# Performance work log

Hardware: AMD Instinct MI355X
Metric: run time of the kernel (lower is better)

The kernel has to match this reference:

```python
import jax, jax.numpy as jnp
import numpy as np

B, NZ, L = 8, 16, 512
E, DM, NH, HD = 256, 512, 16, 32
FF, NL, E1D, PDIM, PMAX = 1024, 8, 32, 64, 24
EPS_LN = 1e-5
EPS_D = 1e-12


def _ln(x, g, b):
    m = jnp.mean(x, axis=-1, keepdims=True)
    v = jnp.mean((x - m) ** 2, axis=-1, keepdims=True)
    return (x - m) / jnp.sqrt(v + EPS_LN) * g + b


def setup_inputs() -> dict:
    key = jax.random.key(0)
    ks = iter(jax.random.split(key, 32))
    rn = lambda shape, fan: jax.random.normal(next(ks), shape, jnp.float32) / np.float32(np.sqrt(fan))
    inp = {
        "z": jax.random.normal(next(ks), (B, NZ, L), jnp.float32),
        "x": jax.random.uniform(next(ks), (B, 20, L), jnp.float32),
        # embeddings
        "pos_table": rn((2 * PMAX + 1, PDIM), 1.0),
        "aa_table": rn((20, E1D), 1.0),
        # embed_x: Linear(nz,E), relu, Linear(E,E)
        "ex_w1": rn((NZ, E), NZ), "ex_b1": jnp.zeros((E,), jnp.float32),
        "ex_w2": rn((E, E), E), "ex_b2": jnp.zeros((E,), jnp.float32),
        # per-layer stacked params
        "Wq": rn((NL, E, DM), E), "Wk": rn((NL, E, DM), E), "Wv": rn((NL, E, DM), E),
        "Wo": rn((NL, DM, E), DM), "bo": jnp.zeros((NL, E), jnp.float32),
        "W2d": rn((NL, PDIM, NH), PDIM), "b2d": jnp.zeros((NL, NH), jnp.float32),
        "W1": rn((NL, E + E1D, FF), E + E1D), "b1": jnp.zeros((NL, FF), jnp.float32),
        "W2": rn((NL, FF, E), FF), "b2": jnp.zeros((NL, E), jnp.float32),
        "g1": jnp.ones((NL, E), jnp.float32), "be1": jnp.zeros((NL, E), jnp.float32),
        "g2": jnp.ones((NL, E), jnp.float32), "be2": jnp.zeros((NL, E), jnp.float32),
        # mlp_3d: Linear(E,E), relu, Linear(E,3)
        "m3_w1": rn((E, E), E), "m3_b1": jnp.zeros((E,), jnp.float32),
        "m3_w2": rn((E, 3), E), "m3_b2": jnp.zeros((3,), jnp.float32),
    }
    return inp


def reference(z, x, pos_table, aa_table, ex_w1, ex_b1, ex_w2, ex_b2,
              Wq, Wk, Wv, Wo, bo, W2d, b2d, W1, b1, W2, b2,
              g1, be1, g2, be2, m3_w1, m3_b1, m3_w2, m3_b2):
    Bn, _, Ln = z.shape
    h = jnp.transpose(z, (0, 2, 1))  # (B, L, nz)
    # relative-position bins: argmin over integer bins == clip to [-PMAX, PMAX]
    rel = jnp.arange(Ln)[None, :] - jnp.arange(Ln)[:, None]
    bins = jnp.clip(rel, -PMAX, PMAX) + PMAX
    pe = pos_table[bins]  # (L, L, PDIM), batch-replicated
    e_aa = aa_table[jnp.argmax(x, axis=1)]  # (B, L, E1D)
    # embed_x MLP
    h = jax.nn.relu(h @ ex_w1 + ex_b1) @ ex_w2 + ex_b2  # (B, L, E)
    scale = np.float32(1.0 / np.sqrt(DM))  # dp_attn_norm='d_model'
    for i in range(NL):
        q = (h @ Wq[i]).reshape(Bn, Ln, NH, HD) * scale
        k = (h @ Wk[i]).reshape(Bn, Ln, NH, HD)
        v = (h @ Wv[i]).reshape(Bn, Ln, NH, HD)
        # learned pairwise bias: mlp_2d then transpose(1,3).transpose(2,3) -> bias[h,i,j] = out[i,j,h]
        bias = jnp.einsum('lmp,ph->hlm', pe, W2d[i]) + b2d[i][:, None, None]
        scores = jnp.einsum('blhd,bmhd->bhlm', q, k) + bias[None]
        attn = jax.nn.softmax(scores, axis=-1)
        o = jnp.einsum('bhlm,bmhd->blhd', attn, v).reshape(Bn, Ln, DM)
        h = _ln(h + (o @ Wo[i] + bo[i]), g1[i], be1[i])
        um = jnp.concatenate([h, e_aa], axis=-1)  # (B, L, E+E1D)
        s2 = jax.nn.relu(um @ W1[i] + b1[i]) @ W2[i] + b2[i]
        h = _ln(h + s2, g2[i], be2[i])
    r = jax.nn.relu(h @ m3_w1 + m3_b1) @ m3_w2 + m3_b2  # (B, L, 3)
    # distance map (get_coords=False path)
    d = jnp.sqrt(jnp.sum((r[:, None, :, :] - r[:, :, None, :]) ** 2, axis=-1) + EPS_D)
    return d  # (B, L, L)
```

## Files before the change

kernel.cpp:

```cpp
#include <hip/hip_runtime.h>
#include <math.h>

constexpr int Bn = 8, NZ = 16, Ln = 512;
constexpr int E = 256, DM = 512, NH = 16, HD = 32;
constexpr int FF = 1024, NL = 8, E1D = 32, PDIM = 64, PMAX = 24;
constexpr int ROWS = Bn * Ln;
constexpr float QSCALE = 0.04419417382415922f;

typedef __attribute__((ext_vector_type(8))) short bf16x8;
typedef __attribute__((ext_vector_type(4))) float floatx4;

__device__ inline unsigned short f2b(float f) {
  union { float f; unsigned u; } v; v.f = f;
  unsigned r = (v.u + 0x7FFF + ((v.u >> 16) & 1)) >> 16;
  return (unsigned short)r;
}
__device__ inline float b2f(unsigned short u) {
  union { unsigned u; float f; } v; v.u = ((unsigned)u) << 16; return v.f;
}

__device__ inline void gll16(const void* g, void* l) {
  __builtin_amdgcn_global_load_lds(
      (const __attribute__((address_space(1))) void*)g,
      (__attribute__((address_space(3))) void*)l, 16, 0, 0);
}

template<int CTRL>
__device__ inline float fmax_dpp(float x) {
  int y = __builtin_amdgcn_update_dpp(0, __float_as_int(x), CTRL, 0xf, 0xf, true);
  return fmaxf(x, __int_as_float(y));
}

template<int CTRL>
__device__ inline float fadd_dpp(float x) {
  int y = __builtin_amdgcn_update_dpp(0, __float_as_int(x), CTRL, 0xf, 0xf, true);
  return x + __int_as_float(y);
}

__global__ __launch_bounds__(256) void transpose_qkv(
    const float* __restrict__ Wq, const float* __restrict__ Wk,
    const float* __restrict__ Wv, unsigned short* __restrict__ qkvT)
{
  __shared__ float t[32][33];
  int zb = blockIdx.z;
  int which = zb / NL, l = zb % NL;
  const float* s = (which == 0 ? Wq : which == 1 ? Wk : Wv) + (size_t)l * E * DM;
  unsigned short* d = qkvT + (size_t)l * 3 * DM * E + (size_t)which * DM * E;
  int c0 = blockIdx.x * 32, r0 = blockIdx.y * 32;
  int tx = threadIdx.x & 31, ty = threadIdx.x >> 5;
  #pragma unroll
  for (int i = 0; i < 4; ++i)
    t[ty + i * 8][tx] = s[(size_t)(r0 + ty + i * 8) * DM + c0 + tx];
  __syncthreads();
  #pragma unroll
  for (int i = 0; i < 4; ++i)
    d[(size_t)(c0 + ty + i * 8) * E + r0 + tx] = f2b(t[tx][ty + i * 8]);
}

__global__ __launch_bounds__(256) void transpose_bf16(
    const float* __restrict__ src, unsigned short* __restrict__ dst,
    int R, int C, size_t sls, size_t dls)
{
  __shared__ float t[32][33];
  int l = blockIdx.z;
  int c0 = blockIdx.x * 32, r0 = blockIdx.y * 32;
  int tx = threadIdx.x & 31, ty = threadIdx.x >> 5;
  const float* s = src + (size_t)l * sls;
  unsigned short* d = dst + (size_t)l * dls;
  #pragma unroll
  for (int i = 0; i < 4; ++i)
    t[ty + i * 8][tx] = s[(size_t)(r0 + ty + i * 8) * C + c0 + tx];
  __syncthreads();
  #pragma unroll
  for (int i = 0; i < 4; ++i)
    d[(size_t)(c0 + ty + i * 8) * R + r0 + tx] = f2b(t[tx][ty + i * 8]);
}

__global__ __launch_bounds__(256) void embed1_kernel(
    const float* __restrict__ z, const float* __restrict__ x,
    const float* __restrict__ aa,
    const float* __restrict__ w1, const float* __restrict__ b1,
    float* __restrict__ t0, unsigned short* __restrict__ umb)
{
  int row = blockIdx.x;
  int b = row >> 9, l = row & (Ln - 1);
  int t = threadIdx.x;
  __shared__ float zs[NZ];
  __shared__ int am_s;
  if (t < NZ) zs[t] = z[((size_t)b * NZ + t) * Ln + l];
  if (t == 0) {
    const float* xp = x + (size_t)b * 20 * Ln + l;
    int am = 0; float bv = xp[0];
    for (int c = 1; c < 20; ++c) { float vv = xp[(size_t)c * Ln]; if (vv > bv) { bv = vv; am = c; } }
    am_s = am;
  }
  __syncthreads();
  float a1 = b1[t];
  #pragma unroll
  for (int nz = 0; nz < NZ; ++nz) a1 += zs[nz] * w1[nz * E + t];
  t0[(size_t)row * E + t] = fmaxf(a1, 0.f);
  if (t < E1D) umb[(size_t)row * (E + E1D) + E + t] = f2b(aa[am_s * E1D + t]);
}

__global__ __launch_bounds__(256) void bias_kernel(
    const float* __restrict__ pos, const float* __restrict__ W2d,
    const float* __restrict__ b2d, float* __restrict__ bias49)
{
  int layer = blockIdx.x;
  for (int idx = threadIdx.x; idx < NH * 49; idx += 256) {
    int hh = idx / 49, bin = idx % 49;
    float acc = b2d[layer * NH + hh];
    for (int p = 0; p < PDIM; ++p)
      acc += pos[bin * PDIM + p] * W2d[((size_t)layer * PDIM + p) * NH + hh];
    bias49[(size_t)layer * NH * 49 + hh * 49 + bin] = acc;
  }
}

template<int BM, int BN, int BK, bool BIAS, bool RELU, bool OUTBF16, bool QKV>
__global__ __launch_bounds__(256) void gemm_mfma(
    const unsigned short* __restrict__ A, const unsigned short* __restrict__ Bt,
    const float* __restrict__ bias,
    float* __restrict__ Cf, unsigned short* __restrict__ Cb, int N, int K)
{
  constexpr int MT = BM / 32, NT = BN / 32;
  const int tid = threadIdx.x;
  const int wave = tid >> 6, ln = tid & 63;
  const int quad = ln >> 4, l16 = ln & 15;
  const int wm = wave >> 1, wn = wave & 1;
  const int m0 = blockIdx.y * BM, n0 = blockIdx.x * BN;

  floatx4 acc[MT][NT] = {};

  if constexpr (BK == 32) {
    __shared__ __align__(16) unsigned short As[2][BM][32];
    __shared__ __align__(16) unsigned short Bs[2][BN][32];
    const int lrow = ln >> 2, chunk = ln & 3;
    const int schunk = chunk ^ ((lrow >> 1) & 3);
    const unsigned short* aSrc = A + (size_t)(m0 + wave * 16 + lrow) * K + schunk * 8;
    const unsigned short* bSrc = Bt + (size_t)(n0 + wave * 16 + lrow) * K + schunk * 8;
    const int rkey = (l16 >> 1) & 3;
    const int nk = K >> 5;

    #pragma unroll
    for (int it = 0; it < BM / 64; ++it)
      gll16(aSrc + (size_t)it * 64 * K, &As[0][it * 64 + wave * 16][0]);
    #pragma unroll
    for (int it = 0; it < BN / 64; ++it)
      gll16(bSrc + (size_t)it * 64 * K, &Bs[0][it * 64 + wave * 16][0]);

    for (int t = 0; t < nk; ++t) {
      const int cur = t & 1;
      __syncthreads();
      if (t + 1 < nk) {
        const int kb = (t + 1) << 5;
        #pragma unroll
        for (int it = 0; it < BM / 64; ++it)
          gll16(aSrc + (size_t)it * 64 * K + kb, &As[cur ^ 1][it * 64 + wave * 16][0]);
        #pragma unroll
        for (int it = 0; it < BN / 64; ++it)
          gll16(bSrc + (size_t)it * 64 * K + kb, &Bs[cur ^ 1][it * 64 + wave * 16][0]);
      }
      bf16x8 af[MT], bfr[NT];
      #pragma unroll
      for (int i = 0; i < MT; ++i)
        af[i] = *(const bf16x8*)&As[cur][wm * (BM / 2) + i * 16 + l16][(quad ^ rkey) * 8];
      #pragma unroll
      for (int j = 0; j < NT; ++j)
        bfr[j] = *(const bf16x8*)&Bs[cur][wn * (BN / 2) + j * 16 + l16][(quad ^ rkey) * 8];
      #pragma unroll
      for (int i = 0; i < MT; ++i)
        #pragma unroll
        for (int j = 0; j < NT; ++j)
          acc[i][j] = __builtin_amdgcn_mfma_f32_16x16x32_bf16(af[i], bfr[j], acc[i][j], 0, 0, 0);
    }
  } else {
    __shared__ __align__(16) unsigned short As[BM][128];
    __shared__ __align__(16) unsigned short Bs[BN][128];
    const int lrow = ln >> 4, chunk = ln & 15;
    const int key = wave * 4 + lrow;
    const int schunk = chunk ^ key;
    const unsigned short* aSrc = A + (size_t)(m0 + key) * K + schunk * 8;
    const unsigned short* bSrc = Bt + (size_t)(n0 + key) * K + schunk * 8;

    for (int kb = 0; kb < K; kb += 128) {
      __syncthreads();
      #pragma unroll
      for (int it = 0; it < BM / 16; ++it)
        gll16(aSrc + (size_t)(it * 16) * K + kb, &As[it * 16 + wave * 4][0]);
      #pragma unroll
      for (int it = 0; it < BN / 16; ++it)
        gll16(bSrc + (size_t)(it * 16) * K + kb, &Bs[it * 16 + wave * 4][0]);
      __syncthreads();
      #pragma unroll
      for (int kc = 0; kc < 4; ++kc) {
        bf16x8 af[MT], bfr[NT];
        #pragma unroll
        for (int i = 0; i < MT; ++i)
          af[i] = *(const bf16x8*)&As[wm * (BM / 2) + i * 16 + l16][(((kc * 4 + quad) ^ l16) * 8)];
        #pragma unroll
        for (int j = 0; j < NT; ++j)
          bfr[j] = *(const bf16x8*)&Bs[wn * (BN / 2) + j * 16 + l16][(((kc * 4 + quad) ^ l16) * 8)];
        #pragma unroll
        for (int i = 0; i < MT; ++i)
          #pragma unroll
          for (int j = 0; j < NT; ++j)
            acc[i][j] = __builtin_amdgcn_mfma_f32_16x16x32_bf16(af[i], bfr[j], acc[i][j], 0, 0, 0);
      }
    }
  }

  #pragma unroll
  for (int i = 0; i < MT; ++i)
    #pragma unroll
    for (int j = 0; j < NT; ++j) {
      int col = n0 + wn * (BN / 2) + j * 16 + l16;
      float bv = BIAS ? bias[col] : 0.f;
      float sc = QKV ? (col < 512 ? QSCALE : 1.f) : 1.f;
      #pragma unroll
      for (int r = 0; r < 4; ++r) {
        int rowg = m0 + wm * (BM / 2) + i * 16 + quad * 4 + r;
        float v = acc[i][j][r] * sc + bv;
        if (RELU) v = fmaxf(v, 0.f);
        if (OUTBF16) Cb[(size_t)rowg * N + col] = f2b(v);
        else Cf[(size_t)rowg * N + col] = v;
      }
    }
}

__global__ __launch_bounds__(256) void gemm_ln(
    const unsigned short* __restrict__ A, const unsigned short* __restrict__ Bt,
    const float* __restrict__ bias, float* __restrict__ h,
    const float* __restrict__ g, const float* __restrict__ be,
    unsigned short* __restrict__ outb, int bstride, int K)
{
  __shared__ __align__(16) unsigned short As[2][16][128];
  __shared__ __align__(16) unsigned short Bs[2][256][128];
  __shared__ __align__(16) float vtile[16][260];
  const int tid = threadIdx.x;
  const int w = tid >> 6, ln = tid & 63;
  const int quad = ln >> 4, l16 = ln & 15;
  const int m0 = blockIdx.x * 16;
  const int lrow = ln >> 4, chunk = ln & 15;
  const int key = w * 4 + lrow;
  const int schunk = chunk ^ key;
  const unsigned short* aSrc = A + (size_t)(m0 + key) * K + schunk * 8;
  const unsigned short* bSrc = Bt + (size_t)key * K + schunk * 8;

  floatx4 acc[4] = {};
  const int nk = K >> 7;

  gll16(aSrc, &As[0][w * 4][0]);
  #pragma unroll
  for (int it = 0; it < 16; ++it)
    gll16(bSrc + (size_t)(it * 16) * K, &Bs[0][it * 16 + w * 4][0]);

  for (int t = 0; t < nk; ++t) {
    const int cur = t & 1;
    __syncthreads();
    if (t + 1 < nk) {
      const int kb = (t + 1) << 7;
      gll16(aSrc + kb, &As[cur ^ 1][w * 4][0]);
      #pragma unroll
      for (int it = 0; it < 16; ++it)
        gll16(bSrc + (size_t)(it * 16) * K + kb, &Bs[cur ^ 1][it * 16 + w * 4][0]);
    }
    #pragma unroll
    for (int kc = 0; kc < 4; ++kc) {
      bf16x8 af = *(const bf16x8*)&As[cur][l16][(((kc * 4 + quad) ^ l16) * 8)];
      #pragma unroll
      for (int nt = 0; nt < 4; ++nt) {
        bf16x8 bf = *(const bf16x8*)&Bs[cur][w * 64 + nt * 16 + l16][(((kc * 4 + quad) ^ l16) * 8)];
        acc[nt] = __builtin_amdgcn_mfma_f32_16x16x32_bf16(af, bf, acc[nt], 0, 0, 0);
      }
    }
  }

  #pragma unroll
  for (int nt = 0; nt < 4; ++nt) {
    int col = w * 64 + nt * 16 + l16;
    float bv = bias[col];
    #pragma unroll
    for (int r = 0; r < 4; ++r) {
      int row = quad * 4 + r;
      vtile[row][col] = acc[nt][r] + bv + h[(size_t)(m0 + row) * E + col];
    }
  }
  __syncthreads();

  const int c0 = ln * 4;
  #pragma unroll
  for (int rr = 0; rr < 4; ++rr) {
    const int lr = w * 4 + rr;
    float4 v = *(const float4*)&vtile[lr][c0];
    float s = v.x + v.y + v.z + v.w;
    float s2 = v.x * v.x + v.y * v.y + v.z * v.z + v.w * v.w;
    s  = fadd_dpp<0xB1>(s);   s  = fadd_dpp<0x4E>(s);
    s2 = fadd_dpp<0xB1>(s2);  s2 = fadd_dpp<0x4E>(s2);
    #pragma unroll
    for (int off = 4; off < 64; off <<= 1) {
      s += __shfl_xor(s, off, 64);
      s2 += __shfl_xor(s2, off, 64);
    }
    const float mean = s * (1.f / E);
    const float rstd = rsqrtf(s2 * (1.f / E) - mean * mean + 1e-5f);
    const float4 gv = *(const float4*)(g + c0);
    const float4 bv = *(const float4*)(be + c0);
    float4 y;
    y.x = (v.x - mean) * rstd * gv.x + bv.x;
    y.y = (v.y - mean) * rstd * gv.y + bv.y;
    y.z = (v.z - mean) * rstd * gv.z + bv.z;
    y.w = (v.w - mean) * rstd * gv.w + bv.w;
    const size_t row = (size_t)(m0 + lr);
    *(float4*)(h + row * E + c0) = y;
    ushort4 yb;
    yb.x = f2b(y.x); yb.y = f2b(y.y); yb.z = f2b(y.z); yb.w = f2b(y.w);
    *(ushort4*)(outb + row * (size_t)bstride + c0) = yb;
  }
}

__global__ __launch_bounds__(256) void attn_kernel(
    const unsigned short* __restrict__ qkv, const float* __restrict__ bias49,
    unsigned short* __restrict__ o)
{
  const int id = blockIdx.x;
  const int bh = ((id >> 6) << 3) | (id & 7);
  const int i0 = ((id >> 3) & 7) * 64;
  const int b = bh >> 4, hh = bh & 15;
  const int tid = threadIdx.x;
  const int wave = tid >> 6, ln = tid & 63;
  const int quad = ln >> 4, l16 = ln & 15;

  __shared__ __align__(16) unsigned short Kt[2][64][40];
  __shared__ __align__(16) unsigned short Vt[2][32][72];
  __shared__ __align__(16) unsigned short Pw[4][2][16][72];
  __shared__ float bsh[49];

  if (tid < 49) bsh[tid] = bias49[hh * 49 + tid];

  const unsigned short* qkvb = qkv + (size_t)b * Ln * 1536;

  const int qrow = i0 + wave * 16 + l16;
  const bf16x8 qf = *(const bf16x8*)(qkvb + (size_t)qrow * 1536 + hh * 32 + quad * 8);

  float m[4], l[4];
  #pragma unroll
  for (int r = 0; r < 4; ++r) { m[r] = -1e30f; l[r] = 0.f; }
  floatx4 acc_o[2] = {};

  const int krow = tid >> 2, kch = (tid & 3) * 8;
  const int vkey = tid & 63, vch = (tid >> 6) * 8;
  const unsigned short* kp = qkvb + (size_t)krow * 1536 + 512 + hh * 32 + kch;
  const unsigned short* vp = qkvb + (size_t)vkey * 1536 + 1024 + hh * 32 + vch;

  float4 kreg = *(const float4*)kp;
  bf16x8 vreg = *(const bf16x8*)vp;

  for (int jt = 0; jt < 8; ++jt) {
    const int j0 = jt * 64;
    const int cur = jt & 1;
    *(float4*)&Kt[cur][krow][kch] = kreg;
    #pragma unroll
    for (int i = 0; i < 8; ++i) Vt[cur][vch + i][vkey] = (unsigned short)vreg[i];
    __syncthreads();
    if (jt < 7) {
      kreg = *(const float4*)(kp + (size_t)(j0 + 64) * 1536);
      vreg = *(const bf16x8*)(vp + (size_t)(j0 + 64) * 1536);
    }

    floatx4 s4[4];
    #pragma unroll
    for (int t = 0; t < 4; ++t) {
      bf16x8 kf = *(const bf16x8*)&Kt[cur][16 * t + l16][quad * 8];
      s4[t] = __builtin_amdgcn_mfma_f32_16x16x32_bf16(qf, kf, (floatx4){0.f, 0.f, 0.f, 0.f}, 0, 0, 0);
    }
    const int relmin = j0 - (i0 + 63), relmax = j0 + 63 - i0;
    if (relmin >= PMAX) {
      float bc = bsh[48];
      #pragma unroll
      for (int t = 0; t < 4; ++t)
        #pragma unroll
        for (int r = 0; r < 4; ++r) s4[t][r] += bc;
    } else if (relmax <= -PMAX) {
      float bc = bsh[0];
      #pragma unroll
      for (int t = 0; t < 4; ++t)
        #pragma unroll
        for (int r = 0; r < 4; ++r) s4[t][r] += bc;
    } else {
      const int base_rel = (j0 + l16) - (i0 + wave * 16 + quad * 4);
      #pragma unroll
      for (int t = 0; t < 4; ++t)
        #pragma unroll
        for (int r = 0; r < 4; ++r) {
          int rel = base_rel + 16 * t - r;
          rel = rel < -PMAX ? -PMAX : (rel > PMAX ? PMAX : rel);
          s4[t][r] += bsh[rel + PMAX];
        }
    }

    float mloc[4], alpha[4], psum[4];
    #pragma unroll
    for (int r = 0; r < 4; ++r) {
      mloc[r] = fmaxf(fmaxf(s4[0][r], s4[1][r]), fmaxf(s4[2][r], s4[3][r]));
      mloc[r] = fmax_dpp<0xB1>(mloc[r]);
      mloc[r] = fmax_dpp<0x4E>(mloc[r]);
      mloc[r] = fmax_dpp<0x124>(mloc[r]);
      mloc[r] = fmax_dpp<0x128>(mloc[r]);
      float mnew = fmaxf(m[r], mloc[r]);
      alpha[r] = __expf(m[r] - mnew);
      m[r] = mnew;
      psum[r] = 0.f;
    }
    #pragma unroll
    for (int t = 0; t < 4; ++t)
      #pragma unroll
      for (int r = 0; r < 4; ++r) {
        float p = __expf(s4[t][r] - m[r]);
        s4[t][r] = p;
        psum[r] += p;
      }
    #pragma unroll
    for (int r = 0; r < 4; ++r) {
      psum[r] = fadd_dpp<0xB1>(psum[r]);
      psum[r] = fadd_dpp<0x4E>(psum[r]);
      #pragma unroll
      for (int off = 4; off < 16; off <<= 1)
        psum[r] += __shfl_xor(psum[r], off, 64);
      l[r] = l[r] * alpha[r] + psum[r];
      acc_o[0][r] *= alpha[r];
      acc_o[1][r] *= alpha[r];
    }

    #pragma unroll
    for (int t = 0; t < 4; ++t)
      #pragma unroll
      for (int r = 0; r < 4; ++r) {
        float p = s4[t][r];
        unsigned short hi = f2b(p);
        unsigned short lo = f2b(p - b2f(hi));
        Pw[wave][0][quad * 4 + r][16 * t + l16] = hi;
        Pw[wave][1][quad * 4 + r][16 * t + l16] = lo;
      }

    #pragma unroll
    for (int kh = 0; kh < 2; ++kh) {
      bf16x8 phi = *(const bf16x8*)&Pw[wave][0][l16][kh * 32 + quad * 8];
      bf16x8 plo = *(const bf16x8*)&Pw[wave][1][l16][kh * 32 + quad * 8];
      #pragma unroll
      for (int nt = 0; nt < 2; ++nt) {
        bf16x8 vf = *(const bf16x8*)&Vt[cur][nt * 16 + l16][kh * 32 + quad * 8];
        acc_o[nt] = __builtin_amdgcn_mfma_f32_16x16x32_bf16(phi, vf, acc_o[nt], 0, 0, 0);
        acc_o[nt] = __builtin_amdgcn_mfma_f32_16x16x32_bf16(plo, vf, acc_o[nt], 0, 0, 0);
      }
    }
  }

  #pragma unroll
  for (int r = 0; r < 4; ++r) {
    float inv = 1.f / l[r];
    size_t rowg = (size_t)b * Ln + i0 + wave * 16 + quad * 4 + r;
    #pragma unroll
    for (int nt = 0; nt < 2; ++nt)
      o[rowg * 512 + hh * 32 + nt * 16 + l16] = f2b(acc_o[nt][r] * inv);
  }
}

template<bool RELU, bool BIAS, bool MIRROR>
__global__ __launch_bounds__(256) void gemm64f(
    const float* __restrict__ A, const float* __restrict__ B,
    const float* __restrict__ bias, float* __restrict__ C,
    unsigned short* __restrict__ mir, int N, int K)
{
  __shared__ __align__(16) float As[16][64];
  __shared__ __align__(16) float Bss[16][68];
  const int tid = threadIdx.x;
  const int tx = tid & 15, ty = tid >> 4;
  const int m0 = blockIdx.y * 64, n0 = blockIdx.x * 64;
  const int arow = tid >> 2, acol = (tid & 3) * 4;
  const int brow = tid >> 6, bcol = tid & 63;
  float acc[4][4] = {};
  for (int kb = 0; kb < K; kb += 16) {
    __syncthreads();
    float4 av = *(const float4*)(A + (size_t)(m0 + arow) * K + kb + acol);
    As[acol + 0][arow] = av.x; As[acol + 1][arow] = av.y;
    As[acol + 2][arow] = av.z; As[acol + 3][arow] = av.w;
    #pragma unroll
    for (int kk = 0; kk < 4; ++kk)
      Bss[brow + kk * 4][bcol] = B[(size_t)(kb + brow + kk * 4) * N + n0 + bcol];
    __syncthreads();
    #pragma unroll
    for (int k = 0; k < 16; ++k) {
      float4 a = *(const float4*)&As[k][4 * ty];
      float4 b = *(const float4*)&Bss[k][4 * tx];
      float av4[4] = {a.x, a.y, a.z, a.w};
      float bv4[4] = {b.x, b.y, b.z, b.w};
      #pragma unroll
      for (int ii = 0; ii < 4; ++ii)
        #pragma unroll
        for (int jj = 0; jj < 4; ++jj)
          acc[ii][jj] += av4[ii] * bv4[jj];
    }
  }
  #pragma unroll
  for (int ii = 0; ii < 4; ++ii) {
    size_t row = (size_t)m0 + 4 * ty + ii;
    int col = n0 + 4 * tx;
    float4 vv;
    vv.x = acc[ii][0]; vv.y = acc[ii][1]; vv.z = acc[ii][2]; vv.w = acc[ii][3];
    if (BIAS) {
      float4 bb = *(const float4*)(bias + col);
      vv.x += bb.x; vv.y += bb.y; vv.z += bb.z; vv.w += bb.w;
    }
    if (RELU) {
      vv.x = fmaxf(vv.x, 0.f); vv.y = fmaxf(vv.y, 0.f);
      vv.z = fmaxf(vv.z, 0.f); vv.w = fmaxf(vv.w, 0.f);
    }
    *(float4*)(C + row * N + col) = vv;
    if (MIRROR) {
      ushort4 mv;
      mv.x = f2b(vv.x); mv.y = f2b(vv.y); mv.z = f2b(vv.z); mv.w = f2b(vv.w);
      *(ushort4*)(mir + row * N + col) = mv;
    }
  }
}

__global__ __launch_bounds__(256) void final_r_kernel(
    const float* __restrict__ t1, const float* __restrict__ w2,
    const float* __restrict__ b2, float* __restrict__ r)
{
  int row = blockIdx.x, t = threadIdx.x;
  float xv = t1[(size_t)row * E + t];
  float p0 = xv * w2[t * 3 + 0];
  float p1 = xv * w2[t * 3 + 1];
  float p2 = xv * w2[t * 3 + 2];
  #pragma unroll
  for (int off = 32; off > 0; off >>= 1) {
    p0 += __shfl_down(p0, off, 64);
    p1 += __shfl_down(p1, off, 64);
    p2 += __shfl_down(p2, off, 64);
  }
  __shared__ float red[4][3];
  if ((t & 63) == 0) { int w = t >> 6; red[w][0] = p0; red[w][1] = p1; red[w][2] = p2; }
  __syncthreads();
  if (t < 3)
    r[(size_t)row * 3 + t] = red[0][t] + red[1][t] + red[2][t] + red[3][t] + b2[t];
}

__global__ __launch_bounds__(512) void dist_kernel(
    const float* __restrict__ r, float* __restrict__ out)
{
  int bi = blockIdx.x;
  int j = threadIdx.x;
  int b = bi >> 9;
  float x0 = r[(size_t)bi * 3 + 0];
  float y0 = r[(size_t)bi * 3 + 1];
  float z0 = r[(size_t)bi * 3 + 2];
  const float* rj = r + ((size_t)b * Ln + j) * 3;
  float dx = rj[0] - x0, dy = rj[1] - y0, dz = rj[2] - z0;
  out[(size_t)bi * Ln + j] = sqrtf(dx * dx + dy * dy + dz * dz + 1e-12f);
}

extern "C" void kernel_launch(void* const* d_in, const int* in_sizes, int n_in,
                              void* d_out, int out_size, void* d_ws, size_t ws_size,
                              hipStream_t stream)
{
  const float* z     = (const float*)d_in[0];
  const float* x     = (const float*)d_in[1];
  const float* pos   = (const float*)d_in[2];
  const float* aa    = (const float*)d_in[3];
  const float* ex_w1 = (const float*)d_in[4];
  const float* ex_b1 = (const float*)d_in[5];
  const float* ex_w2 = (const float*)d_in[6];
  const float* ex_b2 = (const float*)d_in[7];
  const float* Wq    = (const float*)d_in[8];
  const float* Wk    = (const float*)d_in[9];
  const float* Wv    = (const float*)d_in[10];
  const float* Wo    = (const float*)d_in[11];
  const float* bo    = (const float*)d_in[12];
  const float* W2d   = (const float*)d_in[13];
  const float* b2d   = (const float*)d_in[14];
  const float* W1    = (const float*)d_in[15];
  const float* b1    = (const float*)d_in[16];
  const float* W2    = (const float*)d_in[17];
  const float* b2    = (const float*)d_in[18];
  const float* g1    = (const float*)d_in[19];
  const float* be1   = (const float*)d_in[20];
  const float* g2    = (const float*)d_in[21];
  const float* be2   = (const float*)d_in[22];
  const float* m3w1  = (const float*)d_in[23];
  const float* m3b1  = (const float*)d_in[24];
  const float* m3w2  = (const float*)d_in[25];
  const float* m3b2  = (const float*)d_in[26];

  float* ws     = (float*)d_ws;
  float* h      = ws;
  float* t0     = h + (size_t)ROWS * E;
  float* r      = t0 + (size_t)ROWS * E;
  float* bias49 = r + (size_t)ROWS * 3;
  unsigned short* us = (unsigned short*)(bias49 + NL * NH * 49);
  unsigned short* hb   = us;
  unsigned short* umb  = hb  + (size_t)ROWS * E;
  unsigned short* qkvb = umb + (size_t)ROWS * (E + E1D);
  unsigned short* ob   = qkvb + (size_t)ROWS * 3 * DM;
  unsigned short* t1b  = ob  + (size_t)ROWS * DM;
  unsigned short* qkvT = t1b + (size_t)ROWS * FF;
  unsigned short* WoT  = qkvT + (size_t)NL * 3 * DM * E;
  unsigned short* W1T  = WoT  + (size_t)NL * E * DM;
  unsigned short* W2T  = W1T  + (size_t)NL * FF * (E+E1D);
  float* t1f = (float*)t1b;

  transpose_qkv<<<dim3(DM/32, E/32, 3*NL), 256, 0, stream>>>(Wq, Wk, Wv, qkvT);
  transpose_bf16<<<dim3(E/32, DM/32, NL), 256, 0, stream>>>(
      Wo, WoT, DM, E, (size_t)DM * E, (size_t)DM * E);
  transpose_bf16<<<dim3(FF/32, (E+E1D)/32, NL), 256, 0, stream>>>(
      W1, W1T, E + E1D, FF, (size_t)(E+E1D) * FF, (size_t)(E+E1D) * FF);
  transpose_bf16<<<dim3(E/32, FF/32, NL), 256, 0, stream>>>(
      W2, W2T, FF, E, (size_t)FF * E, (size_t)FF * E);

  embed1_kernel<<<ROWS, 256, 0, stream>>>(z, x, aa, ex_w1, ex_b1, t0, umb);
  gemm64f<false,true,true><<<dim3(E/64, ROWS/64), 256, 0, stream>>>(
      t0, ex_w2, ex_b2, h, hb, E, E);
  bias_kernel<<<NL, 256, 0, stream>>>(pos, W2d, b2d, bias49);

  for (int i = 0; i < NL; ++i) {
    gemm_mfma<64,128,128,false,false,true,true><<<dim3(12, 64), 256, 0, stream>>>(
        hb, qkvT + (size_t)i * 3 * DM * E, nullptr, nullptr, qkvb, 3 * DM, E);
    attn_kernel<<<dim3(1024), 256, 0, stream>>>(
        qkvb, bias49 + (size_t)i * NH * 49, ob);
    gemm_ln<<<ROWS/16, 256, 0, stream>>>(
        ob, WoT + (size_t)i * DM * E, bo + (size_t)i * E, h,
        g1 + (size_t)i * E, be1 + (size_t)i * E, umb, E + E1D, DM);
    gemm_mfma<64,64,32,true,true,true,false><<<dim3(FF/64, ROWS/64), 256, 0, stream>>>(
        umb, W1T + (size_t)i * FF * (E+E1D), b1 + (size_t)i * FF, nullptr, t1b, FF, E + E1D);
    gemm_ln<<<ROWS/16, 256, 0, stream>>>(
        t1b, W2T + (size_t)i * E * FF, b2 + (size_t)i * E, h,
        g2 + (size_t)i * E, be2 + (size_t)i * E, hb, E, FF);
  }

  gemm64f<true,true,false><<<dim3(E/64, ROWS/64), 256, 0, stream>>>(
      h, m3w1, m3b1, t1f, nullptr, E, E);
  final_r_kernel<<<ROWS, 256, 0, stream>>>(t1f, m3w2, m3b2, r);
  dist_kernel<<<ROWS, 512, 0, stream>>>(r, (float*)d_out);
}
```

Measured before the change: 749.9 us.

## Double-buffer QKV GEMM with 64-wide K tiles and async prefetch

Replaces the single-buffered 128-wide K tile path of the MFMA GEMM with a double-buffered 64-wide K tile path. The next tile is fetched via global_load_lds while the current one is consumed, which removes one barrier per iteration and overlaps loads with MFMA work. The XOR swizzle changes to 8 chunks per row. The QKV projection launch now selects this path. LDS use stays about the same, but the loop has twice as many iterations, and the prefetch into the other buffer depends on the single barrier for correctness.

```diff
diff --git a/kernel.cpp b/kernel.cpp
--- a/kernel.cpp
+++ b/kernel.cpp
@@ -174,32 +174,43 @@
           acc[i][j] = __builtin_amdgcn_mfma_f32_16x16x32_bf16(af[i], bfr[j], acc[i][j], 0, 0, 0);
     }
   } else {
-    __shared__ __align__(16) unsigned short As[BM][128];
-    __shared__ __align__(16) unsigned short Bs[BN][128];
-    const int lrow = ln >> 4, chunk = ln & 15;
-    const int key = wave * 4 + lrow;
-    const int schunk = chunk ^ key;
-    const unsigned short* aSrc = A + (size_t)(m0 + key) * K + schunk * 8;
-    const unsigned short* bSrc = Bt + (size_t)(n0 + key) * K + schunk * 8;
-
-    for (int kb = 0; kb < K; kb += 128) {
+    __shared__ __align__(16) unsigned short As[2][BM][64];
+    __shared__ __align__(16) unsigned short Bs[2][BN][64];
+    const int lrow = ln >> 3, chunk = ln & 7;
+    const int schunk = chunk ^ lrow;
+    const unsigned short* aSrc = A + (size_t)(m0 + wave * 8 + lrow) * K + schunk * 8;
+    const unsigned short* bSrc = Bt + (size_t)(n0 + wave * 8 + lrow) * K + schunk * 8;
+    const int rkey8 = l16 & 7;
+    const int nk = K >> 6;
+
+    #pragma unroll
+    for (int it = 0; it < BM / 32; ++it)
+      gll16(aSrc + (size_t)(it * 32) * K, &As[0][it * 32 + wave * 8][0]);
+    #pragma unroll
+    for (int it = 0; it < BN / 32; ++it)
+      gll16(bSrc + (size_t)(it * 32) * K, &Bs[0][it * 32 + wave * 8][0]);
+
+    for (int t = 0; t < nk; ++t) {
+      const int cur = t & 1;
       __syncthreads();
-      #pragma unroll
-      for (int it = 0; it < BM / 16; ++it)
-        gll16(aSrc + (size_t)(it * 16) * K + kb, &As[it * 16 + wave * 4][0]);
-      #pragma unroll
-      for (int it = 0; it < BN / 16; ++it)
-        gll16(bSrc + (size_t)(it * 16) * K + kb, &Bs[it * 16 + wave * 4][0]);
-      __syncthreads();
-      #pragma unroll
-      for (int kc = 0; kc < 4; ++kc) {
+      if (t + 1 < nk) {
+        const int kb = (t + 1) << 6;
+        #pragma unroll
+        for (int it = 0; it < BM / 32; ++it)
+          gll16(aSrc + (size_t)(it * 32) * K + kb, &As[cur ^ 1][it * 32 + wave * 8][0]);
+        #pragma unroll
+        for (int it = 0; it < BN / 32; ++it)
+          gll16(bSrc + (size_t)(it * 32) * K + kb, &Bs[cur ^ 1][it * 32 + wave * 8][0]);
+      }
+      #pragma unroll
+      for (int kc = 0; kc < 2; ++kc) {
         bf16x8 af[MT], bfr[NT];
         #pragma unroll
         for (int i = 0; i < MT; ++i)
-          af[i] = *(const bf16x8*)&As[wm * (BM / 2) + i * 16 + l16][(((kc * 4 + quad) ^ l16) * 8)];
+          af[i] = *(const bf16x8*)&As[cur][wm * (BM / 2) + i * 16 + l16][(((kc * 4 + quad) ^ rkey8) * 8)];
         #pragma unroll
         for (int j = 0; j < NT; ++j)
-          bfr[j] = *(const bf16x8*)&Bs[wn * (BN / 2) + j * 16 + l16][(((kc * 4 + quad) ^ l16) * 8)];
+          bfr[j] = *(const bf16x8*)&Bs[cur][wn * (BN / 2) + j * 16 + l16][(((kc * 4 + quad) ^ rkey8) * 8)];
         #pragma unroll
         for (int i = 0; i < MT; ++i)
           #pragma unroll
@@ -623,7 +634,7 @@
   bias_kernel<<<NL, 256, 0, stream>>>(pos, W2d, b2d, bias49);
 
   for (int i = 0; i < NL; ++i) {
-    gemm_mfma<64,128,128,false,false,true,true><<<dim3(12, 64), 256, 0, stream>>>(
+    gemm_mfma<64,128,64,false,false,true,true><<<dim3(12, 64), 256, 0, stream>>>(
         hb, qkvT + (size_t)i * 3 * DM * E, nullptr, nullptr, qkvb, 3 * DM, E);
     attn_kernel<<<dim3(1024), 256, 0, stream>>>(
         qkvb, bias49 + (size_t)i * NH * 49, ob);
```

Result: no change. 759.6 us (+1.3%).
